# Kernel optimization log

Hardware: AMD Instinct MI355X
Metric: run time of the kernel (lower is better)

Reference implementation:

```python
import jax, jax.numpy as jnp
import numpy as np
from jax import lax

KSIZE = 3
EPS_MASK = 1e-6
EPS_BN = 1e-5
DN = ('NCHW', 'OIHW', 'NCHW')
PAD = [(1, 1), (1, 1)]  # (k-1)*dilation//2 = 1 for k=3, d=1


def setup_inputs() -> dict:
    key = jax.random.key(0)
    kx, km, kw, kb = jax.random.split(key, 4)
    N, Cin, Cout, H, W_ = 8, 64, 128, 256, 256
    x = jax.random.normal(kx, (N, Cin, H, W_), dtype=jnp.float32)
    mask = (jax.random.uniform(km, (N, Cin, H, W_)) > 0.25).astype(jnp.float32)
    W = jax.random.normal(kw, (Cout, Cin, KSIZE, KSIZE), dtype=jnp.float32) * 0.05
    b = jax.random.normal(kb, (Cout,), dtype=jnp.float32) * 0.05
    gamma = jnp.ones((Cout,), dtype=jnp.float32)
    beta = jnp.zeros((Cout,), dtype=jnp.float32)
    return {"x": x, "mask": mask, "W": W, "b": b, "gamma": gamma, "beta": beta}


def reference(x, mask, W, b, gamma, beta):
    Cout, Cin = W.shape[0], W.shape[1]
    slide_winsize = float(Cin * KSIZE * KSIZE)

    # Mask-update conv: all-ones (Cout,Cin,k,k) kernel is identical across output
    # channels -> compute once with a single output channel and broadcast.
    ones_k = jnp.ones((1, Cin, KSIZE, KSIZE), dtype=mask.dtype)
    update = lax.conv_general_dilated(mask, ones_k, (1, 1), PAD,
                                      dimension_numbers=DN)  # [N,1,H,W]
    mask_ratio = slide_winsize / (update + EPS_MASK)
    update = jnp.clip(update, 0.0, 1.0)
    mask_ratio = mask_ratio * update

    # Dense conv on masked input
    raw = lax.conv_general_dilated(x * mask, W, (1, 1), PAD,
                                   dimension_numbers=DN)  # [N,Cout,H,W]
    bv = b[None, :, None, None]
    raw = raw + bv
    out = ((raw - bv) * mask_ratio + bv) * update

    # BatchNorm2d (training mode: batch statistics over N,H,W)
    mean = out.mean(axis=(0, 2, 3), keepdims=True)
    var = out.var(axis=(0, 2, 3), keepdims=True)
    out = (out - mean) * lax.rsqrt(var + EPS_BN)
    out = out * gamma[None, :, None, None] + beta[None, :, None, None]

    out = jax.nn.relu(out)
    update_full = jnp.broadcast_to(update, out.shape)  # matches torch [N,Cout,H,W]
    return out, update_full
```

## Files before the change

kernel.cpp:

```cpp
#include <hip/hip_runtime.h>

typedef __attribute__((ext_vector_type(8))) short bf16x8;
typedef __attribute__((ext_vector_type(8))) unsigned short u16x8;
typedef __attribute__((ext_vector_type(4))) float f32x4;
typedef unsigned int u32;

#define CI 64
#define CO 128
#define HH 256
#define WW 256
#define HP 258
#define WP 258
#define SLIDE 576.0f

__device__ __forceinline__ unsigned short f2bf(float f) {
  union { float f; unsigned int u; } c; c.f = f;
  unsigned int u = c.u;
  return (unsigned short)((u + 0x7FFFu + ((u >> 16) & 1u)) >> 16);
}
__device__ __forceinline__ float bf2f(unsigned short h) {
  union { unsigned int u; float f; } c; c.u = ((unsigned int)h) << 16;
  return c.f;
}

__global__ __launch_bounds__(256) void k_xm(const f32x4* __restrict__ x4,
                                            const f32x4* __restrict__ m4,
                                            unsigned short* __restrict__ xm,
                                            float4* __restrict__ msum4,
                                            const float* __restrict__ W,
                                            unsigned short* __restrict__ Wb) {
  __shared__ __align__(16) float tile[64 * 64 + 256];
  int b = blockIdx.x;
  int t = threadIdx.x;
  if (b >= 8192) {
    int blk = b - 8192;
    if (blk < 288) {
      int i = blk * 256 + t;
      int ci = i & 63, co = (i >> 6) & 127, tap = i >> 13;
      int kh = tap / 3, kw = tap - 3 * (tap / 3);
      Wb[i] = f2bf(W[((co * CI + ci) * 3 + kh) * 3 + kw]);
    } else {
      int i = (blk - 288) * 256 + t;
      if (i >= 8 * 1028) return;
      int n = i / 1028, p = i - n * 1028;
      int hh, wp;
      if (p < 258) { hh = 0; wp = p; }
      else if (p < 516) { hh = 257; wp = p - 258; }
      else { int q = p - 516; hh = 1 + (q >> 1); wp = (q & 1) * 257; }
      u16x8 z = {0, 0, 0, 0, 0, 0, 0, 0};
      unsigned short* d = xm + (((size_t)n * HP + hh) * WP + wp) * CI;
#pragma unroll
      for (int k = 0; k < 8; ++k) *(u16x8*)(d + k * 8) = z;
    }
    return;
  }
  int wt = b & 3, h = (b >> 2) & 255, n = b >> 10;
  int w0 = wt * 64;
  int p4 = t & 15, chg = t >> 4;
  size_t base = (size_t)n * CI * 16384 + (size_t)h * 64 + (w0 >> 2) + p4;
  float msx = 0.f, msy = 0.f, msz = 0.f, msw = 0.f;
#pragma unroll
  for (int j = 0; j < 4; ++j) {
    int ch = chg * 4 + j;
    size_t o = base + (size_t)ch * 16384;
    f32x4 xv = __builtin_nontemporal_load(&x4[o]);
    f32x4 mv = __builtin_nontemporal_load(&m4[o]);
    msx += mv.x; msy += mv.y; msz += mv.z; msw += mv.w;
    f32x4 pr = xv * mv;
    int kk = (ch >> 3) & 3;
    *(f32x4*)&tile[ch * 64 + ((p4 * 4) ^ (kk << 2))] = pr;
  }
  msx += __shfl_xor(msx, 16); msy += __shfl_xor(msy, 16);
  msz += __shfl_xor(msz, 16); msw += __shfl_xor(msw, 16);
  msx += __shfl_xor(msx, 32); msy += __shfl_xor(msy, 32);
  msz += __shfl_xor(msz, 32); msw += __shfl_xor(msw, 32);
  int wave = t >> 6, lane = t & 63;
  float4* red = (float4*)&tile[4096];
  if (lane < 16) red[wave * 16 + lane] = make_float4(msx, msy, msz, msw);
  __syncthreads();
  size_t dstb = (((size_t)n * HP + h + 1) * WP + (w0 + 1)) * CI;
#pragma unroll
  for (int iter = 0; iter < 2; ++iter) {
    int c = iter * 256 + t;
    int px = c >> 3, cg = c & 7;
    u16x8 v;
#pragma unroll
    for (int e = 0; e < 8; ++e) {
      int ch = cg * 8 + e;
      int kk = (ch >> 3) & 3;
      v[e] = f2bf(tile[ch * 64 + (px ^ (kk << 2))]);
    }
    *(u16x8*)(xm + dstb + (size_t)px * CI + cg * 8) = v;
  }
  if (t < 16) {
    float4 a = red[t], b2 = red[16 + t], c2 = red[32 + t], d2 = red[48 + t];
    float4 s;
    s.x = a.x + b2.x + c2.x + d2.x; s.y = a.y + b2.y + c2.y + d2.y;
    s.z = a.z + b2.z + c2.z + d2.z; s.w = a.w + b2.w + c2.w + d2.w;
    msum4[(size_t)n * 16384 + (size_t)h * 64 + (w0 >> 2) + t] = s;
  }
}

__global__ __launch_bounds__(512) void k_conv(
    const unsigned short* __restrict__ xm, const unsigned short* __restrict__ Wb,
    const float* __restrict__ msum, const float* __restrict__ bias,
    unsigned short* __restrict__ blob, float* __restrict__ psum, float* __restrict__ psq,
    float* __restrict__ upd) {
  __shared__ __align__(16) char lds[51472];
  int b = blockIdx.x;
  int work = (b & 7) * 512 + (b >> 3);
  int wt = work & 1, h = (work >> 1) & 255, n = work >> 9;
  int w0 = wt * 128;
  int t = threadIdx.x;
  int lane = t & 63, wave = t >> 6;
  float* lr = (float*)(lds + 49920);
  float* lu = (float*)(lds + 50432);
  float* cs = (float*)(lds + 50944);
#pragma unroll
  for (int iter = 0; iter < 6; ++iter) {
    int c = iter * 512 + t;
    int r = (c >= 2080) ? 2 : (c >= 1040 ? 1 : 0);
    int cc = c - r * 1040;
    int wslot = cc >> 3, sub = cc & 7;
    int srcc = (wslot << 3) + (sub ^ (wslot & 7));
    const unsigned short* g = xm + (((size_t)n * HP + h + r) * WP + w0) * CI + (size_t)srcc * 8;
    u32 ldsoff = (u32)((iter * 512 + (wave << 6)) << 4);
    __builtin_amdgcn_global_load_lds((const __attribute__((address_space(1))) u32*)g,
        (__attribute__((address_space(3))) u32*)(void*)(lds + ldsoff), 16, 0, 0);
  }
  if (t < 48) {
    int c = 3072 + t;
    int cc = c - 2080;
    int wslot = cc >> 3, sub = cc & 7;
    int srcc = (wslot << 3) + (sub ^ (wslot & 7));
    const unsigned short* g = xm + (((size_t)n * HP + h + 2) * WP + w0) * CI + (size_t)srcc * 8;
    u32 ldsoff = (u32)(3072 << 4);
    __builtin_amdgcn_global_load_lds((const __attribute__((address_space(1))) u32*)g,
        (__attribute__((address_space(3))) u32*)(void*)(lds + ldsoff), 16, 0, 0);
  }
  if (t < 130) {
    int w = w0 - 1 + t;
    float s = 0.f;
    if ((unsigned)w < 256u) {
      const float* mcol = msum + (size_t)n * 65536 + w;
      if (h >= 1) s += mcol[(h - 1) * 256];
      s += mcol[h * 256];
      if (h < 255) s += mcol[(h + 1) * 256];
    }
    cs[t] = s;
  }
  __syncthreads();
  if (t < 128) {
    float s = cs[t] + cs[t + 1] + cs[t + 2];
    float uc = fminf(s, 1.0f);
    lu[t] = uc;
    lr[t] = SLIDE / (s + 1e-6f) * uc;
  }

  int wm = wave >> 2, wn = wave & 3;
  int l15 = lane & 15, l4 = lane >> 4;
  f32x4 zero = {0.f, 0.f, 0.f, 0.f};
  f32x4 acc[4][2];
#pragma unroll
  for (int i = 0; i < 4; ++i)
#pragma unroll
    for (int j = 0; j < 2; ++j) acc[i][j] = zero;

#pragma unroll
  for (int kh = 0; kh < 3; ++kh) {
#pragma unroll
    for (int kw = 0; kw < 3; ++kw) {
      const unsigned short* wtap = Wb + ((kh * 3 + kw) * CO + wn * 32) * CI;
#pragma unroll
      for (int ks = 0; ks < 2; ++ks) {
        bf16x8 af[4], bfr[2];
#pragma unroll
        for (int mf = 0; mf < 4; ++mf) {
          int wslot = wm * 64 + mf * 16 + l15 + kw;
          int baddr = (((kh * 130 + wslot) << 7) + ks * 64 + l4 * 16) ^ ((wslot & 7) << 4);
          af[mf] = *(const bf16x8*)(lds + baddr);
        }
#pragma unroll
        for (int nf = 0; nf < 2; ++nf)
          bfr[nf] = *(const bf16x8*)(wtap + (nf * 16 + l15) * CI + ks * 32 + l4 * 8);
#pragma unroll
        for (int mf = 0; mf < 4; ++mf)
#pragma unroll
          for (int nf = 0; nf < 2; ++nf)
            acc[mf][nf] = __builtin_amdgcn_mfma_f32_16x16x32_bf16(af[mf], bfr[nf], acc[mf][nf], 0, 0, 0);
      }
    }
  }
  __syncthreads();

  float bv[2];
#pragma unroll
  for (int nf = 0; nf < 2; ++nf) bv[nf] = bias[wn * 32 + nf * 16 + l15];
  float rs_s[2] = {0.f, 0.f}, rq_s[2] = {0.f, 0.f};
  int px0 = wm * 64 + l4 * 4;
#pragma unroll
  for (int mf = 0; mf < 4; ++mf) {
    int pxb = px0 + mf * 16;
    float rs0 = lr[pxb], rs1 = lr[pxb + 1], rs2 = lr[pxb + 2], rs3 = lr[pxb + 3];
    float uc0 = lu[pxb], uc1 = lu[pxb + 1], uc2 = lu[pxb + 2], uc3 = lu[pxb + 3];
#pragma unroll
    for (int nf = 0; nf < 2; ++nf) {
      int co = wn * 32 + nf * 16 + l15;
      float v0 = acc[mf][nf][0] * rs0 + bv[nf] * uc0;
      float v1 = acc[mf][nf][1] * rs1 + bv[nf] * uc1;
      float v2 = acc[mf][nf][2] * rs2 + bv[nf] * uc2;
      float v3 = acc[mf][nf][3] * rs3 + bv[nf] * uc3;
      unsigned short h0 = f2bf(v0), h1 = f2bf(v1), h2 = f2bf(v2), h3 = f2bf(v3);
      float w0f = bf2f(h0), w1f = bf2f(h1), w2f = bf2f(h2), w3f = bf2f(h3);
      rs_s[nf] += w0f + w1f + w2f + w3f;
      rq_s[nf] += w0f * w0f + w1f * w1f + w2f * w2f + w3f * w3f;
      u32 lo = (u32)h0 | ((u32)h1 << 16);
      u32 hi = (u32)h2 | ((u32)h3 << 16);
      *(uint2*)(lds + co * 272 + (wm << 7) + (mf * 16 + l4 * 4) * 2) = make_uint2(lo, hi);
    }
  }
  float* sred = (float*)(lds + 34816);
#pragma unroll
  for (int nf = 0; nf < 2; ++nf) {
    float s = rs_s[nf], q = rq_s[nf];
    s += __shfl_xor(s, 16); s += __shfl_xor(s, 32);
    q += __shfl_xor(q, 16); q += __shfl_xor(q, 32);
    if (l4 == 0) {
      sred[(wave * 2 + nf) * 16 + l15] = s;
      sred[256 + (wave * 2 + nf) * 16 + l15] = q;
    }
  }
  __syncthreads();
  int pixrow = (n * CO) << 16;
#pragma unroll
  for (int iter = 0; iter < 4; ++iter) {
    int i = iter * 512 + t;
    int co = i >> 4, oct = i & 15;
    u16x8 v = *(const u16x8*)(lds + co * 272 + oct * 16);
    *(u16x8*)(blob + (size_t)(pixrow + (co << 16) + (h << 8) + w0 + oct * 8)) = v;
  }
  float* updp = upd + (((size_t)(n * CO)) << 16) + (h << 8) + w0;
#pragma unroll
  for (int iter = 0; iter < 8; ++iter) {
    int i = iter * 512 + t;
    int co = i >> 5, seg = i & 31;
    f32x4 uv = *(const f32x4*)&lu[seg * 4];
    __builtin_nontemporal_store(uv, (f32x4*)(updp + ((size_t)co << 16) + seg * 4));
  }
  int co = t & 127;
  int wnq = co >> 5, nf2 = (co >> 4) & 1, cc2 = co & 15;
  int r0 = ((wnq) * 2 + nf2) * 16 + cc2;
  int r1 = ((4 + wnq) * 2 + nf2) * 16 + cc2;
  float a0 = sred[r0] + sred[r1];
  float a1 = sred[256 + r0] + sred[256 + r1];
  if (t < 128) psum[(size_t)b * 128 + co] = a0;
  else if (t < 256) psq[(size_t)b * 128 + co] = a1;
}

__global__ void k_bnstats(const float* __restrict__ psum, const float* __restrict__ psq,
                          const float* __restrict__ gamma, const float* __restrict__ beta,
                          float* __restrict__ bn_scale, float* __restrict__ bn_shift) {
  int co = blockIdx.x;
  int t = threadIdx.x;
  float s = 0.f, q = 0.f;
  for (int i = t; i < 4096; i += 256) {
    s += psum[(size_t)i * 128 + co];
    q += psq[(size_t)i * 128 + co];
  }
#pragma unroll
  for (int o = 1; o < 64; o <<= 1) { s += __shfl_xor(s, o); q += __shfl_xor(q, o); }
  __shared__ float red[8];
  int wv = t >> 6, ln = t & 63;
  if (ln == 0) { red[wv] = s; red[4 + wv] = q; }
  __syncthreads();
  if (t == 0) {
    s = red[0] + red[1] + red[2] + red[3];
    q = red[4] + red[5] + red[6] + red[7];
    const float inv = 1.0f / 524288.0f;
    float mean = s * inv;
    float var = q * inv - mean * mean;
    float sc = gamma[co] * rsqrtf(var + 1e-5f);
    bn_scale[co] = sc;
    bn_shift[co] = beta[co] - mean * sc;
  }
}

__global__ __launch_bounds__(256) void k_out(const unsigned short* __restrict__ blob,
                                             const float* __restrict__ bn_scale,
                                             const float* __restrict__ bn_shift,
                                             float* __restrict__ out) {
  int b = blockIdx.x;
  int h = b & 255, n = b >> 8;
  int t = threadIdx.x;
  size_t rowbase = ((size_t)(n * CO) << 16) + (h << 8);
#pragma unroll
  for (int iter = 0; iter < 32; ++iter) {
    int i = iter * 256 + t;
    int c = i >> 6, q = i & 63;
    size_t off = rowbase + ((size_t)c << 16) + q * 4;
    uint2 raw = *(const uint2*)(blob + off);
    float sc = bn_scale[c], sh = bn_shift[c];
    f32x4 v;
    v.x = fmaxf(bf2f((unsigned short)(raw.x & 0xFFFF)) * sc + sh, 0.f);
    v.y = fmaxf(bf2f((unsigned short)(raw.x >> 16)) * sc + sh, 0.f);
    v.z = fmaxf(bf2f((unsigned short)(raw.y & 0xFFFF)) * sc + sh, 0.f);
    v.w = fmaxf(bf2f((unsigned short)(raw.y >> 16)) * sc + sh, 0.f);
    __builtin_nontemporal_store(v, (f32x4*)(out + off));
  }
}

extern "C" void kernel_launch(void* const* d_in, const int* in_sizes, int n_in,
                              void* d_out, int out_size, void* d_ws, size_t ws_size,
                              hipStream_t stream) {
  (void)in_sizes; (void)n_in; (void)out_size; (void)ws_size;
  const float* x     = (const float*)d_in[0];
  const float* mask  = (const float*)d_in[1];
  const float* W     = (const float*)d_in[2];
  const float* bias  = (const float*)d_in[3];
  const float* gamma = (const float*)d_in[4];
  const float* beta  = (const float*)d_in[5];

  float* out = (float*)d_out;
  float* upd_out = out + 67108864;

  char* wsb = (char*)d_ws;
  unsigned short* Wb = (unsigned short*)wsb;
  float* msum     = (float*)(wsb + (2u << 20));
  float* bn_scale = (float*)(wsb + (8u << 20));
  float* bn_shift = bn_scale + 128;
  float* part_sum = (float*)(wsb + (9u << 20));
  float* part_sq  = (float*)(wsb + (11u << 20));
  unsigned short* xm   = (unsigned short*)(wsb + (16u << 20));
  unsigned short* blob = (unsigned short*)(wsb + (96u << 20));

  k_xm<<<8513, 256, 0, stream>>>((const f32x4*)x, (const f32x4*)mask, xm,
                                 (float4*)msum, W, Wb);
  k_conv<<<4096, 512, 0, stream>>>(xm, Wb, msum, bias, blob, part_sum, part_sq, upd_out);
  k_bnstats<<<128, 256, 0, stream>>>(part_sum, part_sq, gamma, beta, bn_scale, bn_shift);
  k_out<<<2048, 256, 0, stream>>>(blob, bn_scale, bn_shift, out);
}
```

Before: 312.9 us.

## Recompute convolution in output pass instead of storing bf16 intermediate

Splits the conv into a stats-only pass that no longer writes the bf16 pre-BN tensor, and a second pass that recomputes the convolution and applies batch-norm and ReLU directly from LDS. This removes the large intermediate write and re-read through global memory. In exchange it doubles the MFMA convolution work and input tile loads.

```diff
diff --git a/kernel.cpp b/kernel.cpp
--- a/kernel.cpp
+++ b/kernel.cpp
@@ -101,21 +101,21 @@
   }
 }
 
-__global__ __launch_bounds__(512) void k_conv(
+__global__ __launch_bounds__(512) void k_conv_stats(
     const unsigned short* __restrict__ xm, const unsigned short* __restrict__ Wb,
     const float* __restrict__ msum, const float* __restrict__ bias,
-    unsigned short* __restrict__ blob, float* __restrict__ psum, float* __restrict__ psq,
-    float* __restrict__ upd) {
-  __shared__ __align__(16) char lds[51472];
+    float* __restrict__ psum, float* __restrict__ psq, float* __restrict__ upd) {
+  __shared__ __align__(16) char lds[53520];
   int b = blockIdx.x;
   int work = (b & 7) * 512 + (b >> 3);
   int wt = work & 1, h = (work >> 1) & 255, n = work >> 9;
   int w0 = wt * 128;
   int t = threadIdx.x;
   int lane = t & 63, wave = t >> 6;
-  float* lr = (float*)(lds + 49920);
-  float* lu = (float*)(lds + 50432);
-  float* cs = (float*)(lds + 50944);
+  float* lr   = (float*)(lds + 49920);
+  float* lu   = (float*)(lds + 50432);
+  float* cs   = (float*)(lds + 50944);
+  float* sred = (float*)(lds + 51472);
 #pragma unroll
   for (int iter = 0; iter < 6; ++iter) {
     int c = iter * 512 + t;
@@ -191,8 +191,6 @@
       }
     }
   }
-  __syncthreads();
-
   float bv[2];
 #pragma unroll
   for (int nf = 0; nf < 2; ++nf) bv[nf] = bias[wn * 32 + nf * 16 + l15];
@@ -205,21 +203,16 @@
     float uc0 = lu[pxb], uc1 = lu[pxb + 1], uc2 = lu[pxb + 2], uc3 = lu[pxb + 3];
 #pragma unroll
     for (int nf = 0; nf < 2; ++nf) {
-      int co = wn * 32 + nf * 16 + l15;
       float v0 = acc[mf][nf][0] * rs0 + bv[nf] * uc0;
       float v1 = acc[mf][nf][1] * rs1 + bv[nf] * uc1;
       float v2 = acc[mf][nf][2] * rs2 + bv[nf] * uc2;
       float v3 = acc[mf][nf][3] * rs3 + bv[nf] * uc3;
-      unsigned short h0 = f2bf(v0), h1 = f2bf(v1), h2 = f2bf(v2), h3 = f2bf(v3);
-      float w0f = bf2f(h0), w1f = bf2f(h1), w2f = bf2f(h2), w3f = bf2f(h3);
+      float w0f = bf2f(f2bf(v0)), w1f = bf2f(f2bf(v1));
+      float w2f = bf2f(f2bf(v2)), w3f = bf2f(f2bf(v3));
       rs_s[nf] += w0f + w1f + w2f + w3f;
       rq_s[nf] += w0f * w0f + w1f * w1f + w2f * w2f + w3f * w3f;
-      u32 lo = (u32)h0 | ((u32)h1 << 16);
-      u32 hi = (u32)h2 | ((u32)h3 << 16);
-      *(uint2*)(lds + co * 272 + (wm << 7) + (mf * 16 + l4 * 4) * 2) = make_uint2(lo, hi);
-    }
-  }
-  float* sred = (float*)(lds + 34816);
+    }
+  }
 #pragma unroll
   for (int nf = 0; nf < 2; ++nf) {
     float s = rs_s[nf], q = rq_s[nf];
@@ -231,14 +224,6 @@
     }
   }
   __syncthreads();
-  int pixrow = (n * CO) << 16;
-#pragma unroll
-  for (int iter = 0; iter < 4; ++iter) {
-    int i = iter * 512 + t;
-    int co = i >> 4, oct = i & 15;
-    u16x8 v = *(const u16x8*)(lds + co * 272 + oct * 16);
-    *(u16x8*)(blob + (size_t)(pixrow + (co << 16) + (h << 8) + w0 + oct * 8)) = v;
-  }
   float* updp = upd + (((size_t)(n * CO)) << 16) + (h << 8) + w0;
 #pragma unroll
   for (int iter = 0; iter < 8; ++iter) {
@@ -285,27 +270,137 @@
   }
 }
 
-__global__ __launch_bounds__(256) void k_out(const unsigned short* __restrict__ blob,
-                                             const float* __restrict__ bn_scale,
-                                             const float* __restrict__ bn_shift,
-                                             float* __restrict__ out) {
+__global__ __launch_bounds__(512) void k_conv_out(
+    const unsigned short* __restrict__ xm, const unsigned short* __restrict__ Wb,
+    const float* __restrict__ msum, const float* __restrict__ bias,
+    const float* __restrict__ bn_scale, const float* __restrict__ bn_shift,
+    float* __restrict__ out) {
+  __shared__ __align__(16) char lds[52496];
   int b = blockIdx.x;
-  int h = b & 255, n = b >> 8;
+  int work = (b & 7) * 512 + (b >> 3);
+  int wt = work & 1, h = (work >> 1) & 255, n = work >> 9;
+  int w0 = wt * 128;
   int t = threadIdx.x;
-  size_t rowbase = ((size_t)(n * CO) << 16) + (h << 8);
-#pragma unroll
-  for (int iter = 0; iter < 32; ++iter) {
-    int i = iter * 256 + t;
-    int c = i >> 6, q = i & 63;
-    size_t off = rowbase + ((size_t)c << 16) + q * 4;
-    uint2 raw = *(const uint2*)(blob + off);
-    float sc = bn_scale[c], sh = bn_shift[c];
+  int lane = t & 63, wave = t >> 6;
+  float* lr  = (float*)(lds + 49920);
+  float* lu  = (float*)(lds + 50432);
+  float* cs  = (float*)(lds + 50944);
+  float* lsc = (float*)(lds + 51472);
+  float* lsh = (float*)(lds + 51984);
+#pragma unroll
+  for (int iter = 0; iter < 6; ++iter) {
+    int c = iter * 512 + t;
+    int r = (c >= 2080) ? 2 : (c >= 1040 ? 1 : 0);
+    int cc = c - r * 1040;
+    int wslot = cc >> 3, sub = cc & 7;
+    int srcc = (wslot << 3) + (sub ^ (wslot & 7));
+    const unsigned short* g = xm + (((size_t)n * HP + h + r) * WP + w0) * CI + (size_t)srcc * 8;
+    u32 ldsoff = (u32)((iter * 512 + (wave << 6)) << 4);
+    __builtin_amdgcn_global_load_lds((const __attribute__((address_space(1))) u32*)g,
+        (__attribute__((address_space(3))) u32*)(void*)(lds + ldsoff), 16, 0, 0);
+  }
+  if (t < 48) {
+    int c = 3072 + t;
+    int cc = c - 2080;
+    int wslot = cc >> 3, sub = cc & 7;
+    int srcc = (wslot << 3) + (sub ^ (wslot & 7));
+    const unsigned short* g = xm + (((size_t)n * HP + h + 2) * WP + w0) * CI + (size_t)srcc * 8;
+    u32 ldsoff = (u32)(3072 << 4);
+    __builtin_amdgcn_global_load_lds((const __attribute__((address_space(1))) u32*)g,
+        (__attribute__((address_space(3))) u32*)(void*)(lds + ldsoff), 16, 0, 0);
+  }
+  if (t < 130) {
+    int w = w0 - 1 + t;
+    float s = 0.f;
+    if ((unsigned)w < 256u) {
+      const float* mcol = msum + (size_t)n * 65536 + w;
+      if (h >= 1) s += mcol[(h - 1) * 256];
+      s += mcol[h * 256];
+      if (h < 255) s += mcol[(h + 1) * 256];
+    }
+    cs[t] = s;
+  }
+  if (t >= 256 && t < 384) { int c = t - 256; lsc[c] = bn_scale[c]; lsh[c] = bn_shift[c]; }
+  __syncthreads();
+  if (t < 128) {
+    float s = cs[t] + cs[t + 1] + cs[t + 2];
+    float uc = fminf(s, 1.0f);
+    lu[t] = uc;
+    lr[t] = SLIDE / (s + 1e-6f) * uc;
+  }
+
+  int wm = wave >> 2, wn = wave & 3;
+  int l15 = lane & 15, l4 = lane >> 4;
+  f32x4 zero = {0.f, 0.f, 0.f, 0.f};
+  f32x4 acc[4][2];
+#pragma unroll
+  for (int i = 0; i < 4; ++i)
+#pragma unroll
+    for (int j = 0; j < 2; ++j) acc[i][j] = zero;
+
+#pragma unroll
+  for (int kh = 0; kh < 3; ++kh) {
+#pragma unroll
+    for (int kw = 0; kw < 3; ++kw) {
+      const unsigned short* wtap = Wb + ((kh * 3 + kw) * CO + wn * 32) * CI;
+#pragma unroll
+      for (int ks = 0; ks < 2; ++ks) {
+        bf16x8 af[4], bfr[2];
+#pragma unroll
+        for (int mf = 0; mf < 4; ++mf) {
+          int wslot = wm * 64 + mf * 16 + l15 + kw;
+          int baddr = (((kh * 130 + wslot) << 7) + ks * 64 + l4 * 16) ^ ((wslot & 7) << 4);
+          af[mf] = *(const bf16x8*)(lds + baddr);
+        }
+#pragma unroll
+        for (int nf = 0; nf < 2; ++nf)
+          bfr[nf] = *(const bf16x8*)(wtap + (nf * 16 + l15) * CI + ks * 32 + l4 * 8);
+#pragma unroll
+        for (int mf = 0; mf < 4; ++mf)
+#pragma unroll
+          for (int nf = 0; nf < 2; ++nf)
+            acc[mf][nf] = __builtin_amdgcn_mfma_f32_16x16x32_bf16(af[mf], bfr[nf], acc[mf][nf], 0, 0, 0);
+      }
+    }
+  }
+  __syncthreads();
+
+  float bv[2];
+#pragma unroll
+  for (int nf = 0; nf < 2; ++nf) bv[nf] = bias[wn * 32 + nf * 16 + l15];
+  int px0 = wm * 64 + l4 * 4;
+#pragma unroll
+  for (int mf = 0; mf < 4; ++mf) {
+    int pxb = px0 + mf * 16;
+    float rs0 = lr[pxb], rs1 = lr[pxb + 1], rs2 = lr[pxb + 2], rs3 = lr[pxb + 3];
+    float uc0 = lu[pxb], uc1 = lu[pxb + 1], uc2 = lu[pxb + 2], uc3 = lu[pxb + 3];
+#pragma unroll
+    for (int nf = 0; nf < 2; ++nf) {
+      int co = wn * 32 + nf * 16 + l15;
+      float v0 = acc[mf][nf][0] * rs0 + bv[nf] * uc0;
+      float v1 = acc[mf][nf][1] * rs1 + bv[nf] * uc1;
+      float v2 = acc[mf][nf][2] * rs2 + bv[nf] * uc2;
+      float v3 = acc[mf][nf][3] * rs3 + bv[nf] * uc3;
+      unsigned short h0 = f2bf(v0), h1 = f2bf(v1), h2 = f2bf(v2), h3 = f2bf(v3);
+      u32 lo = (u32)h0 | ((u32)h1 << 16);
+      u32 hi = (u32)h2 | ((u32)h3 << 16);
+      *(uint2*)(lds + co * 272 + pxb * 2) = make_uint2(lo, hi);
+    }
+  }
+  __syncthreads();
+  size_t outb = (((size_t)(n * CO)) << 16) + (h << 8) + w0;
+#pragma unroll
+  for (int iter = 0; iter < 8; ++iter) {
+    int i = iter * 512 + t;
+    int co = i >> 5, q = i & 31;
+    uint2 raw = *(const uint2*)(lds + co * 272 + q * 8);
+    float sc = lsc[co], sh = lsh[co];
     f32x4 v;
     v.x = fmaxf(bf2f((unsigned short)(raw.x & 0xFFFF)) * sc + sh, 0.f);
     v.y = fmaxf(bf2f((unsigned short)(raw.x >> 16)) * sc + sh, 0.f);
     v.z = fmaxf(bf2f((unsigned short)(raw.y & 0xFFFF)) * sc + sh, 0.f);
     v.w = fmaxf(bf2f((unsigned short)(raw.y >> 16)) * sc + sh, 0.f);
-    __builtin_nontemporal_store(v, (f32x4*)(out + off));
+    __builtin_nontemporal_store(v, (f32x4*)(out + outb + ((size_t)co << 16) + q * 4));
   }
 }
 
@@ -330,12 +425,11 @@
   float* bn_shift = bn_scale + 128;
   float* part_sum = (float*)(wsb + (9u << 20));
   float* part_sq  = (float*)(wsb + (11u << 20));
-  unsigned short* xm   = (unsigned short*)(wsb + (16u << 20));
-  unsigned short* blob = (unsigned short*)(wsb + (96u << 20));
+  unsigned short* xm = (unsigned short*)(wsb + (16u << 20));
 
   k_xm<<<8513, 256, 0, stream>>>((const f32x4*)x, (const f32x4*)mask, xm,
                                  (float4*)msum, W, Wb);
-  k_conv<<<4096, 512, 0, stream>>>(xm, Wb, msum, bias, blob, part_sum, part_sq, upd_out);
+  k_conv_stats<<<4096, 512, 0, stream>>>(xm, Wb, msum, bias, part_sum, part_sq, upd_out);
   k_bnstats<<<128, 256, 0, stream>>>(part_sum, part_sq, gamma, beta, bn_scale, bn_shift);
-  k_out<<<2048, 256, 0, stream>>>(blob, bn_scale, bn_shift, out);
-}
+  k_conv_out<<<4096, 512, 0, stream>>>(xm, Wb, msum, bias, bn_scale, bn_shift, out);
+}
```

Result: slower. 412.8 us (+31.9%).
